# Kernel optimization log

Measured on AMD Instinct MI355X. Metric: run time of the kernel, lower is better.

## Reference

```python
import jax, jax.numpy as jnp
import numpy as np

B, N, C = 64, 197, 768
H = 12
N_TOK = 118
CUTOFF = 0.15


def setup_inputs() -> dict:
    key = jax.random.key(0)
    ks = jax.random.split(key, 6)
    s = 0.02
    return {
        "x": jax.random.normal(ks[0], (B, N, C), jnp.float32),
        "ln1_w": jnp.ones((C,), jnp.float32),
        "ln1_b": jnp.zeros((C,), jnp.float32),
        "qkv_w": jax.random.normal(ks[1], (3 * C, C), jnp.float32) * s,
        "proj_w": jax.random.normal(ks[2], (C, C), jnp.float32) * s,
        "proj_b": jnp.zeros((C,), jnp.float32),
        "gamma1": jnp.ones((C,), jnp.float32),
        "ln2_w": jnp.ones((C,), jnp.float32),
        "ln2_b": jnp.zeros((C,), jnp.float32),
        "fc1_w": jax.random.normal(ks[3], (4 * C, C), jnp.float32) * s,
        "fc1_b": jnp.zeros((4 * C,), jnp.float32),
        "fc2_w": jax.random.normal(ks[4], (C, 4 * C), jnp.float32) * s,
        "fc2_b": jnp.zeros((C,), jnp.float32),
        "gamma2": jnp.ones((C,), jnp.float32),
    }


def _ln(x, w, b, eps=1e-5):
    m = x.mean(-1, keepdims=True)
    v = ((x - m) ** 2).mean(-1, keepdims=True)
    return (x - m) / jnp.sqrt(v + eps) * w + b


def _attention(x, qkv_w, proj_w, proj_b):
    Bx, Nx, Cx = x.shape
    dh = Cx // H
    qkv = x @ qkv_w.T                                    # [B,N,3C]
    qk = qkv[:, :, : 2 * Cx].reshape(Bx, Nx, 2, H, dh).transpose(2, 0, 3, 1, 4)
    q, k = qk[0], qk[1]                                  # [B,H,N,dh]
    v = qkv[:, :, 2 * Cx :].reshape(Bx, Nx, H, dh).transpose(0, 2, 1, 3)
    attn = jax.nn.softmax((q * dh ** -0.5) @ k.transpose(0, 1, 3, 2), axis=-1)  # [B,H,N,N]
    out = (attn @ v).transpose(0, 2, 1, 3).reshape(Bx, Nx, Cx)
    return out @ proj_w.T + proj_b, attn


def _selector(x, attn, n_tokens, cutoff):
    # attention-weighted scores
    cls_aw = attn[:, :, 1:, 0].mean(-1)[..., None]        # [B,H,1]
    cls_attn = (attn[:, :, 0, 1:] * cls_aw).mean(1)       # [B,N-1]
    img_aw = attn[:, :, 0, 0][..., None]                  # [B,H,1]
    img_attn = (attn[:, :, 1:, 1:].mean(2) * img_aw).mean(1)
    token_attn = cls_attn + img_attn                      # [B,N-1]
    # FFT low-frequency-energy score (detached in original)
    img_token = jax.lax.stop_gradient(x[:, 1:].astype(jnp.float32).transpose(0, 2, 1))  # [B,C,N-1]
    f = jnp.fft.fft(img_token, axis=-1)
    amp = jnp.abs(f)
    pha = jnp.angle(f)
    L = img_token.shape[-1]
    d0 = (L * cutoff / 2.0) ** 2
    m0 = (L - 1) / 2.0
    grid = jnp.arange(L, dtype=jnp.float32)
    kernel = 1.0 - jnp.exp(-((grid - m0) ** 2) / (2.0 * d0))  # high-pass notch
    amp = amp * kernel
    f2 = amp * jnp.cos(pha) + 1j * amp * jnp.sin(pha)
    tok = jnp.fft.ifft(f2, axis=-1)                       # [B,C,N-1] complex
    token_lfe = jnp.abs(tok).sum(1) / jnp.abs(img_token).sum(1).mean(-1)[..., None]
    scores = token_lfe * token_attn                        # [B,N-1]
    _, idx = jax.lax.top_k(scores, n_tokens)               # [B,n_tokens]
    Cx = x.shape[-1]
    sav = jnp.take_along_axis(x[:, 1:], idx[:, :, None], axis=1)  # [B,n_tokens,C]
    return jnp.concatenate([x[:, 0:1], sav], axis=1)


def reference(x, ln1_w, ln1_b, qkv_w, proj_w, proj_b, gamma1,
              ln2_w, ln2_b, fc1_w, fc1_b, fc2_w, fc2_b, gamma2):
    x_msa, attn = _attention(_ln(x, ln1_w, ln1_b), qkv_w, proj_w, proj_b)
    x = gamma1 * x_msa + x
    x = _selector(x, attn, N_TOK, CUTOFF)                 # [B,1+N_TOK,C]
    h = _ln(x, ln2_w, ln2_b)
    h = jax.nn.gelu(h @ fc1_w.T + fc1_b, approximate=False)
    h = h @ fc2_w.T + fc2_b
    return gamma2 * h + x
```

## Files before the change

kernel.cpp:

```cpp
#include <hip/hip_runtime.h>
#include <math.h>

#define NTOK 197
#define NIMG 196
#define CDIM 768
#define NHEAD 12
#define HD 64
#define BATCH 64
#define NSEL 118
#define ROWS_FULL (BATCH*NTOK)
#define ROWS_SEL  (BATCH*(NSEL+1))

typedef short bf16x8 __attribute__((ext_vector_type(8)));
typedef float f32x4  __attribute__((ext_vector_type(4)));

#define GLDS(g, l) __builtin_amdgcn_global_load_lds( \
    (const __attribute__((address_space(1))) void*)(g), \
    (__attribute__((address_space(3))) void*)(l), 16, 0, 0)

__device__ __forceinline__ unsigned short f2bf(float f){
  union { float f; unsigned u; } v; v.f = f;
  unsigned r = v.u + 0x7FFF + ((v.u >> 16) & 1);
  return (unsigned short)(r >> 16);
}
__device__ __forceinline__ float bf2f(unsigned short h){
  union { unsigned u; float f; } v; v.u = ((unsigned)h) << 16; return v.f;
}

template<int OUT>
__global__ __launch_bounds__(256) void ln_kernel(
    const float* __restrict__ x, const float* __restrict__ w,
    const float* __restrict__ b, void* __restrict__ outv)
{
  const int row = blockIdx.x;
  const int t = threadIdx.x;
  const float* xr = x + (size_t)row * CDIM;
  float v0 = xr[t], v1 = xr[t+256], v2 = xr[t+512];
  float s = v0 + v1 + v2;
  __shared__ float red[4], red2[4];
  #pragma unroll
  for (int o=32;o>0;o>>=1) s += __shfl_down(s,o);
  if ((t&63)==0) red[t>>6] = s;
  __syncthreads();
  const float mean = (red[0]+red[1]+red[2]+red[3]) / 768.0f;
  const float d0=v0-mean, d1=v1-mean, d2=v2-mean;
  float vs = d0*d0 + d1*d1 + d2*d2;
  #pragma unroll
  for (int o=32;o>0;o>>=1) vs += __shfl_down(vs,o);
  if ((t&63)==0) red2[t>>6] = vs;
  __syncthreads();
  const float var = (red2[0]+red2[1]+red2[2]+red2[3]) / 768.0f;
  const float rstd = 1.0f / sqrtf(var + 1e-5f);
  const float o0 = d0*rstd*w[t]     + b[t];
  const float o1 = d1*rstd*w[t+256] + b[t+256];
  const float o2 = d2*rstd*w[t+512] + b[t+512];
  if (OUT == 0){
    float* orow = (float*)outv + (size_t)row * CDIM;
    orow[t] = o0; orow[t+256] = o1; orow[t+512] = o2;
  } else {
    unsigned short* orow = (unsigned short*)outv + (size_t)row * CDIM;
    orow[t] = f2bf(o0); orow[t+256] = f2bf(o1); orow[t+512] = f2bf(o2);
  }
}

__global__ __launch_bounds__(256) void ln_split3_kernel(
    const float* __restrict__ x, const float* __restrict__ w,
    const float* __restrict__ b, unsigned short* __restrict__ dst, size_t plane)
{
  const int row = blockIdx.x;
  const int t = threadIdx.x;
  const float* xr = x + (size_t)row * CDIM;
  float v0 = xr[t], v1 = xr[t+256], v2 = xr[t+512];
  float s = v0 + v1 + v2;
  __shared__ float red[4], red2[4];
  #pragma unroll
  for (int o=32;o>0;o>>=1) s += __shfl_down(s,o);
  if ((t&63)==0) red[t>>6] = s;
  __syncthreads();
  const float mean = (red[0]+red[1]+red[2]+red[3]) / 768.0f;
  const float d0=v0-mean, d1=v1-mean, d2=v2-mean;
  float vs = d0*d0 + d1*d1 + d2*d2;
  #pragma unroll
  for (int o=32;o>0;o>>=1) vs += __shfl_down(vs,o);
  if ((t&63)==0) red2[t>>6] = vs;
  __syncthreads();
  const float var = (red2[0]+red2[1]+red2[2]+red2[3]) / 768.0f;
  const float rstd = 1.0f / sqrtf(var + 1e-5f);
  const float ov[3] = { d0*rstd*w[t]     + b[t],
                        d1*rstd*w[t+256] + b[t+256],
                        d2*rstd*w[t+512] + b[t+512] };
  #pragma unroll
  for (int e=0;e<3;e++){
    const int col = t + e*256;
    const float f = ov[e];
    const unsigned short p0 = f2bf(f);
    const float r1 = f - bf2f(p0);
    const unsigned short p1 = f2bf(r1);
    const unsigned short p2 = f2bf(r1 - bf2f(p1));
    dst[(size_t)row*CDIM + col]             = p0;
    dst[plane + (size_t)row*CDIM + col]     = p1;
    dst[2*plane + (size_t)row*CDIM + col]   = p2;
  }
}

__global__ __launch_bounds__(256) void cvt_bf16_kernel(
    const float* __restrict__ src, unsigned short* __restrict__ dst, int n4)
{
  const int i = blockIdx.x*256 + threadIdx.x;
  if (i < n4){
    const float4 v = *(const float4*)(src + (size_t)i*4);
    dst[(size_t)i*4+0] = f2bf(v.x); dst[(size_t)i*4+1] = f2bf(v.y);
    dst[(size_t)i*4+2] = f2bf(v.z); dst[(size_t)i*4+3] = f2bf(v.w);
  }
}

__global__ __launch_bounds__(192) void cvt3_kernel(
    const float* __restrict__ w, unsigned short* __restrict__ W3, int K)
{
  const int n = blockIdx.x, t = threadIdx.x;
  const float4 v = *(const float4*)(w + (size_t)n*K + t*4);
  ushort4 hi, lo;
  hi.x = f2bf(v.x); lo.x = f2bf(v.x - bf2f(hi.x));
  hi.y = f2bf(v.y); lo.y = f2bf(v.y - bf2f(hi.y));
  hi.z = f2bf(v.z); lo.z = f2bf(v.z - bf2f(hi.z));
  hi.w = f2bf(v.w); lo.w = f2bf(v.w - bf2f(hi.w));
  *(ushort4*)(W3 + (size_t)n*2*K + t*4)     = hi;
  *(ushort4*)(W3 + (size_t)n*2*K + K + t*4) = lo;
}

__global__ __launch_bounds__(256) void cvt_split3_kernel(
    const float* __restrict__ src, unsigned short* __restrict__ dst,
    int n4, size_t plane)
{
  const int i = blockIdx.x*256 + threadIdx.x;
  if (i >= n4) return;
  const float4 v = *(const float4*)(src + (size_t)i*4);
  const float f[4] = {v.x, v.y, v.z, v.w};
  unsigned short p0[4], p1[4], p2[4];
  #pragma unroll
  for (int q=0;q<4;q++){
    p0[q] = f2bf(f[q]);
    const float r1 = f[q] - bf2f(p0[q]);
    p1[q] = f2bf(r1);
    const float r2 = r1 - bf2f(p1[q]);
    p2[q] = f2bf(r2);
  }
  *(ushort4*)(dst + (size_t)i*4)           = make_ushort4(p0[0],p0[1],p0[2],p0[3]);
  *(ushort4*)(dst + plane + (size_t)i*4)   = make_ushort4(p1[0],p1[1],p1[2],p1[3]);
  *(ushort4*)(dst + 2*plane + (size_t)i*4) = make_ushort4(p2[0],p2[1],p2[2],p2[3]);
}

__global__ __launch_bounds__(256) void gemm_f32_kernel(
    const float* __restrict__ A, const float* __restrict__ W,
    float* __restrict__ out, int M, int N, int K)
{
  __shared__ float As[16][132];
  __shared__ float Bs[16][132];
  const int t  = threadIdx.x;
  const int tx = t & 15, ty = t >> 4;
  const int m0 = blockIdx.x * 128, n0 = blockIdx.y * 128;
  const int lr = t >> 2, lc = (t & 3) << 2;
  float acc[2][2][4][4] = {{{{0.f}}}};
  const float4 z4 = make_float4(0.f,0.f,0.f,0.f);
  const int rowA0 = m0 + lr, rowA1 = m0 + 64 + lr;
  const size_t strA0 = (size_t)rowA0 * K, strA1 = (size_t)rowA1 * K;
  const size_t strW0 = (size_t)(n0+lr) * K, strW1 = (size_t)(n0+64+lr) * K;
  for (int k0=0; k0<K; k0+=16){
    float4 a0 = (rowA0 < M) ? *(const float4*)(A + strA0 + k0 + lc) : z4;
    float4 a1 = (rowA1 < M) ? *(const float4*)(A + strA1 + k0 + lc) : z4;
    float4 w0 = *(const float4*)(W + strW0 + k0 + lc);
    float4 w1 = *(const float4*)(W + strW1 + k0 + lc);
    __syncthreads();
    As[lc+0][lr]=a0.x; As[lc+1][lr]=a0.y; As[lc+2][lr]=a0.z; As[lc+3][lr]=a0.w;
    As[lc+0][64+lr]=a1.x; As[lc+1][64+lr]=a1.y; As[lc+2][64+lr]=a1.z; As[lc+3][64+lr]=a1.w;
    Bs[lc+0][lr]=w0.x; Bs[lc+1][lr]=w0.y; Bs[lc+2][lr]=w0.z; Bs[lc+3][lr]=w0.w;
    Bs[lc+0][64+lr]=w1.x; Bs[lc+1][64+lr]=w1.y; Bs[lc+2][64+lr]=w1.z; Bs[lc+3][64+lr]=w1.w;
    __syncthreads();
    #pragma unroll
    for (int k=0;k<16;k++){
      const float4 av0 = *(const float4*)&As[k][ty*4];
      const float4 av1 = *(const float4*)&As[k][64+ty*4];
      const float4 bv0 = *(const float4*)&Bs[k][tx*4];
      const float4 bv1 = *(const float4*)&Bs[k][64+tx*4];
      const float ar[2][4] = {{av0.x,av0.y,av0.z,av0.w},{av1.x,av1.y,av1.z,av1.w}};
      const float br[2][4] = {{bv0.x,bv0.y,bv0.z,bv0.w},{bv1.x,bv1.y,bv1.z,bv1.w}};
      #pragma unroll
      for (int ri=0;ri<2;ri++)
        #pragma unroll
        for (int i=0;i<4;i++)
          #pragma unroll
          for (int ci=0;ci<2;ci++)
            #pragma unroll
            for (int j=0;j<4;j++)
              acc[ri][ci][i][j] = fmaf(ar[ri][i], br[ci][j], acc[ri][ci][i][j]);
    }
  }
  #pragma unroll
  for (int ri=0;ri<2;ri++){
    #pragma unroll
    for (int i=0;i<4;i++){
      const int row = m0 + ri*64 + ty*4 + i;
      if (row >= M) continue;
      #pragma unroll
      for (int ci=0;ci<2;ci++){
        const int col = n0 + ci*64 + tx*4;
        *(float4*)(out + (size_t)row*N + col) =
          make_float4(acc[ri][ci][i][0],acc[ri][ci][i][1],acc[ri][ci][i][2],acc[ri][ci][i][3]);
      }
    }
  }
}

__global__ __launch_bounds__(512) void mfma_gemm6w_kernel(
    const unsigned short* __restrict__ A3, const unsigned short* __restrict__ W3,
    float* __restrict__ out, int M, int N, int K, size_t planeA, size_t planeW,
    int gx)
{
  __shared__ __align__(16) unsigned short As[3][64*64];
  __shared__ __align__(16) unsigned short Ws[256*64];
  const int nwg = gridDim.x;
  const int q8 = nwg >> 3, r8 = nwg & 7;
  const int xcd = blockIdx.x & 7, lid = blockIdx.x >> 3;
  const int swz = (xcd < r8) ? (xcd*(q8+1) + lid) : (r8*(q8+1) + (xcd-r8)*q8 + lid);
  const int bx = swz % gx, by = swz / gx;

  const int t = threadIdx.x;
  const int w = t >> 6, lane = t & 63;
  const int m0 = bx * 64, n0 = by * 256;
  const int wr = w >> 2, wc = w & 3;
  f32x4 acc[2][4];
  #pragma unroll
  for (int i=0;i<2;i++)
    #pragma unroll
    for (int j=0;j<4;j++){ acc[i][j][0]=0.f; acc[i][j][1]=0.f; acc[i][j][2]=0.f; acc[i][j][3]=0.f; }

  const int srow = lane >> 3;
  const int slot = lane & 7;
  const int scol = (slot ^ srow) * 8;
  const int aloc = w*8;
  const int wloc = w*32;
  const int fr = lane & 15;
  const int kg = lane >> 4;

  #define SEGW(NA)                                                            \
    _Pragma("unroll")                                                         \
    for (int ksub = 0; ksub < 2; ksub++){                                     \
      const int kbyte = ksub*64 + kg*16;                                      \
      bf16x8 b[4];                                                            \
      _Pragma("unroll")                                                       \
      for (int ni=0; ni<4; ni++){                                             \
        const int br = wc*64 + ni*16 + fr;                                    \
        b[ni] = *(const bf16x8*)(Ws + br*64 + ((kbyte ^ ((br&7)<<4)) >> 1));  \
      }                                                                       \
      _Pragma("unroll")                                                       \
      for (int p=0; p<NA; p++){                                               \
        bf16x8 a[2];                                                          \
        _Pragma("unroll")                                                     \
        for (int mi=0; mi<2; mi++){                                           \
          const int ar = wr*32 + mi*16 + fr;                                  \
          a[mi] = *(const bf16x8*)(As[p] + ar*64 + ((kbyte ^ ((ar&7)<<4)) >> 1)); \
        }                                                                     \
        _Pragma("unroll")                                                     \
        for (int mi=0; mi<2; mi++)                                            \
          _Pragma("unroll")                                                   \
          for (int ni=0; ni<4; ni++)                                          \
            acc[mi][ni] = __builtin_amdgcn_mfma_f32_16x16x32_bf16(a[mi], b[ni], acc[mi][ni], 0, 0, 0); \
      }                                                                       \
    }

  #define STAGE_W(P)                                                          \
    _Pragma("unroll")                                                         \
    for (int tt=0; tt<4; tt++){                                               \
      const int rl = wloc + tt*8;                                             \
      GLDS(W3 + (size_t)(P)*planeW + (size_t)(n0+rl+srow)*K + k0 + scol, Ws + rl*64); \
    }

  for (int k0 = 0; k0 < K; k0 += 64){
    __syncthreads();
    #pragma unroll
    for (int p=0; p<3; p++)
      GLDS(A3 + (size_t)p*planeA + (size_t)(m0+aloc+srow)*K + k0 + scol, As[p] + aloc*64);
    STAGE_W(0)
    __syncthreads();
    SEGW(3)
    __syncthreads();
    STAGE_W(1)
    __syncthreads();
    SEGW(2)
    __syncthreads();
    STAGE_W(2)
    __syncthreads();
    SEGW(1)
  }
  #undef SEGW
  #undef STAGE_W

  const int cL = lane & 15, rL = lane >> 4;
  #pragma unroll
  for (int mi=0; mi<2; mi++){
    #pragma unroll
    for (int ni=0; ni<4; ni++){
      const int col = n0 + wc*64 + ni*16 + cL;
      const int rowb = m0 + wr*32 + mi*16 + rL*4;
      #pragma unroll
      for (int r=0; r<4; r++){
        const int row = rowb + r;
        if (row >= M) continue;
        out[(size_t)row*N + col] = acc[mi][ni][r];
      }
    }
  }
}

template<int EPI>
__global__ __launch_bounds__(512) void mfma_gemm1w_kernel(
    const unsigned short* __restrict__ A, const unsigned short* __restrict__ W,
    const float* __restrict__ bias, const float* __restrict__ gamma,
    const float* __restrict__ resid, void* __restrict__ outv,
    int M, int N, int K, int gx)
{
  __shared__ __align__(16) unsigned short As[64*64];
  __shared__ __align__(16) unsigned short Ws[256*64];
  const int nwg = gridDim.x;
  const int q8 = nwg >> 3, r8 = nwg & 7;
  const int xcd = blockIdx.x & 7, lid = blockIdx.x >> 3;
  const int swz = (xcd < r8) ? (xcd*(q8+1) + lid) : (r8*(q8+1) + (xcd-r8)*q8 + lid);
  const int bx = swz % gx, by = swz / gx;

  const int t = threadIdx.x;
  const int w = t >> 6, lane = t & 63;
  const int m0 = bx * 64, n0 = by * 256;
  const int wr = w >> 2, wc = w & 3;
  f32x4 acc[2][4];
  #pragma unroll
  for (int i=0;i<2;i++)
    #pragma unroll
    for (int j=0;j<4;j++){ acc[i][j][0]=0.f; acc[i][j][1]=0.f; acc[i][j][2]=0.f; acc[i][j][3]=0.f; }

  const int srow = lane >> 3;
  const int slot = lane & 7;
  const int scol = (slot ^ srow) * 8;
  const int aloc = w*8;
  const int wloc = w*32;
  const int fr = lane & 15;
  const int kg = lane >> 4;

  for (int k0 = 0; k0 < K; k0 += 64){
    __syncthreads();
    GLDS(A + (size_t)(m0+aloc+srow)*K + k0 + scol, As + aloc*64);
    #pragma unroll
    for (int tt=0; tt<4; tt++){
      const int rl = wloc + tt*8;
      GLDS(W + (size_t)(n0+rl+srow)*K + k0 + scol, Ws + rl*64);
    }
    __syncthreads();
    #pragma unroll
    for (int ksub = 0; ksub < 2; ksub++){
      const int kbyte = ksub*64 + kg*16;
      bf16x8 b[4];
      #pragma unroll
      for (int ni=0; ni<4; ni++){
        const int br = wc*64 + ni*16 + fr;
        b[ni] = *(const bf16x8*)(Ws + br*64 + ((kbyte ^ ((br&7)<<4)) >> 1));
      }
      bf16x8 a[2];
      #pragma unroll
      for (int mi=0; mi<2; mi++){
        const int ar = wr*32 + mi*16 + fr;
        a[mi] = *(const bf16x8*)(As + ar*64 + ((kbyte ^ ((ar&7)<<4)) >> 1));
      }
      #pragma unroll
      for (int mi=0; mi<2; mi++)
        #pragma unroll
        for (int ni=0; ni<4; ni++)
          acc[mi][ni] = __builtin_amdgcn_mfma_f32_16x16x32_bf16(a[mi], b[ni], acc[mi][ni], 0, 0, 0);
    }
  }

  const int cL = lane & 15, rL = lane >> 4;
  #pragma unroll
  for (int mi=0; mi<2; mi++){
    #pragma unroll
    for (int ni=0; ni<4; ni++){
      const int col = n0 + wc*64 + ni*16 + cL;
      const int rowb = m0 + wr*32 + mi*16 + rL*4;
      const float bb = bias[col];
      #pragma unroll
      for (int r=0; r<4; r++){
        const int row = rowb + r;
        if (row >= M) continue;
        float v = acc[mi][ni][r] + bb;
        if (EPI == 2){
          v = 0.5f*v*(1.0f + erff(v*0.7071067811865475f));
          ((unsigned short*)outv)[(size_t)row*N + col] = f2bf(v);
        } else {
          v = gamma[col]*v + resid[(size_t)row*N + col];
          ((float*)outv)[(size_t)row*N + col] = v;
        }
      }
    }
  }
}

__global__ __launch_bounds__(512) void mfma_proj3_kernel(
    const unsigned short* __restrict__ A, const unsigned short* __restrict__ W,
    const float* __restrict__ bias, const float* __restrict__ gamma,
    const float* __restrict__ resid, float* __restrict__ out,
    int M, int N, int K, int gx)
{
  __shared__ __align__(16) unsigned short Ah[64*64], Al[64*64];
  __shared__ __align__(16) unsigned short Ws[256*64];
  const int nwg = gridDim.x;
  const int q8 = nwg >> 3, r8 = nwg & 7;
  const int xcd = blockIdx.x & 7, lid = blockIdx.x >> 3;
  const int swz = (xcd < r8) ? (xcd*(q8+1) + lid) : (r8*(q8+1) + (xcd-r8)*q8 + lid);
  const int bx = swz % gx, by = swz / gx;

  const int t = threadIdx.x;
  const int w = t >> 6, lane = t & 63;
  const int m0 = bx * 64, n0 = by * 256;
  const int wr = w >> 2, wc = w & 3;
  const int lda = 2*K;
  f32x4 acc[2][4];
  #pragma unroll
  for (int i=0;i<2;i++)
    #pragma unroll
    for (int j=0;j<4;j++){ acc[i][j][0]=0.f; acc[i][j][1]=0.f; acc[i][j][2]=0.f; acc[i][j][3]=0.f; }

  const int srow = lane >> 3;
  const int slot = lane & 7;
  const int scol = (slot ^ srow) * 8;
  const int aloc = w*8;
  const int wloc = w*32;
  const int fr = lane & 15;
  const int kg = lane >> 4;

  #define PSEG(NA)                                                            \
    _Pragma("unroll")                                                         \
    for (int ksub = 0; ksub < 2; ksub++){                                     \
      const int kbyte = ksub*64 + kg*16;                                      \
      bf16x8 b[4];                                                            \
      _Pragma("unroll")                                                       \
      for (int ni=0; ni<4; ni++){                                             \
        const int br = wc*64 + ni*16 + fr;                                    \
        b[ni] = *(const bf16x8*)(Ws + br*64 + ((kbyte ^ ((br&7)<<4)) >> 1));  \
      }                                                                       \
      _Pragma("unroll")                                                       \
      for (int mi=0; mi<2; mi++){                                             \
        const int ar = wr*32 + mi*16 + fr;                                    \
        const int ao = ar*64 + ((kbyte ^ ((ar&7)<<4)) >> 1);                  \
        bf16x8 ah = *(const bf16x8*)(Ah + ao);                                \
        _Pragma("unroll")                                                     \
        for (int ni=0; ni<4; ni++)                                            \
          acc[mi][ni] = __builtin_amdgcn_mfma_f32_16x16x32_bf16(ah, b[ni], acc[mi][ni], 0, 0, 0); \
        if (NA > 1){                                                          \
          bf16x8 al = *(const bf16x8*)(Al + ao);                              \
          _Pragma("unroll")                                                   \
          for (int ni=0; ni<4; ni++)                                          \
            acc[mi][ni] = __builtin_amdgcn_mfma_f32_16x16x32_bf16(al, b[ni], acc[mi][ni], 0, 0, 0); \
        }                                                                     \
      }                                                                       \
    }

  for (int k0 = 0; k0 < K; k0 += 64){
    __syncthreads();
    {
      const size_t abase = (size_t)(m0+aloc+srow)*lda + k0 + scol;
      GLDS(A + abase,     Ah + aloc*64);
      GLDS(A + abase + K, Al + aloc*64);
    }
    #pragma unroll
    for (int tt=0; tt<4; tt++){
      const int rl = wloc + tt*8;
      GLDS(W + (size_t)(n0+rl+srow)*lda + k0 + scol, Ws + rl*64);
    }
    __syncthreads();
    PSEG(2)
    __syncthreads();
    #pragma unroll
    for (int tt=0; tt<4; tt++){
      const int rl = wloc + tt*8;
      GLDS(W + (size_t)(n0+rl+srow)*lda + K + k0 + scol, Ws + rl*64);
    }
    __syncthreads();
    PSEG(1)
  }
  #undef PSEG

  const int cL = lane & 15, rL = lane >> 4;
  #pragma unroll
  for (int mi=0; mi<2; mi++){
    #pragma unroll
    for (int ni=0; ni<4; ni++){
      const int col = n0 + wc*64 + ni*16 + cL;
      const int rowb = m0 + wr*32 + mi*16 + rL*4;
      const float bb = bias[col];
      const float gg = gamma[col];
      #pragma unroll
      for (int r=0; r<4; r++){
        const int row = rowb + r;
        if (row >= M) continue;
        out[(size_t)row*N + col] = gg*(acc[mi][ni][r] + bb) + resid[(size_t)row*N + col];
      }
    }
  }
}

__global__ __launch_bounds__(256) void attn_flash_kernel(
    const float* __restrict__ qkv, double* __restrict__ mbuf,
    double* __restrict__ lbuf, unsigned short* __restrict__ msa3)
{
  __shared__ float Kt[NTOK][HD];
  __shared__ double q0s[HD];
  __shared__ float m0sh;
  __shared__ double red[4];
  __shared__ float l0f;
  const int bh = blockIdx.x;
  const int b = bh / NHEAD, h = bh % NHEAD;
  const float* basep = qkv + (size_t)b*NTOK*2304 + h*HD;
  for (int li=threadIdx.x; li<NTOK*16; li+=256){
    const int r = li >> 4, c4 = (li & 15) << 2;
    *(float4*)&Kt[r][c4] = *(const float4*)(basep + (size_t)r*2304 + 768 + c4);
  }
  if (threadIdx.x < 16){
    const float4 t4 = *(const float4*)(basep + threadIdx.x*4);
    q0s[threadIdx.x*4+0] = (double)t4.x*0.125; q0s[threadIdx.x*4+1] = (double)t4.y*0.125;
    q0s[threadIdx.x*4+2] = (double)t4.z*0.125; q0s[threadIdx.x*4+3] = (double)t4.w*0.125;
  }
  __syncthreads();
  const int i = threadIdx.x;
  float4 q[16];
  float4 o[16];
  float m = -INFINITY, l = 0.f;
  if (i < NTOK){
    #pragma unroll
    for (int dd=0; dd<16; dd++){
      float4 tq = *(const float4*)(basep + (size_t)i*2304 + dd*4);
      q[dd] = make_float4(tq.x*0.125f, tq.y*0.125f, tq.z*0.125f, tq.w*0.125f);
      o[dd] = make_float4(0.f,0.f,0.f,0.f);
    }
    for (int j=0;j<NTOK;j++){
      float s = 0.f;
      #pragma unroll
      for (int dd=0;dd<16;dd++){
        const float4 kk = *(const float4*)&Kt[j][dd*4];
        s = fmaf(q[dd].x,kk.x,s); s = fmaf(q[dd].y,kk.y,s);
        s = fmaf(q[dd].z,kk.z,s); s = fmaf(q[dd].w,kk.w,s);
      }
      const float mn = fmaxf(m, s);
      const float sc = expf(m - mn);
      const float p  = expf(s - mn);
      l = l*sc + p;
      if (sc != 1.0f){
        #pragma unroll
        for (int dd=0;dd<16;dd++){
          o[dd].x *= sc; o[dd].y *= sc; o[dd].z *= sc; o[dd].w *= sc;
        }
      }
      m = mn;
      const float* vrow = basep + (size_t)j*2304 + 1536;
      #pragma unroll
      for (int dd=0;dd<16;dd++){
        const float4 vv = *(const float4*)(vrow + dd*4);
        o[dd].x = fmaf(p,vv.x,o[dd].x); o[dd].y = fmaf(p,vv.y,o[dd].y);
        o[dd].z = fmaf(p,vv.z,o[dd].z); o[dd].w = fmaf(p,vv.w,o[dd].w);
      }
    }
    mbuf[bh*NTOK+i] = (double)m;
    if (i > 0) lbuf[bh*NTOK+i] = (double)(1.0f/l);
    if (i == 0) m0sh = m;
  }
  __syncthreads();
  double e = 0.0;
  if (i < NTOK){
    double s64 = 0.0;
    #pragma unroll
    for (int d=0; d<HD; d++) s64 = fma(q0s[d], (double)Kt[i][d], s64);
    e = exp(s64 - (double)m0sh);
  }
  #pragma unroll
  for (int o2=32;o2>0;o2>>=1) e += __shfl_down(e,o2);
  if ((i&63)==0) red[i>>6] = e;
  __syncthreads();
  if (i==0){
    const double l0 = 1.0/(red[0]+red[1]+red[2]+red[3]);
    lbuf[bh*NTOK] = l0;
    l0f = (float)l0;
  }
  __syncthreads();
  if (i >= NTOK) return;
  const float linv = (i == 0) ? l0f : (1.0f/l);
  unsigned short* orow = msa3 + ((size_t)b*NTOK + i)*1536 + h*HD;
  #pragma unroll
  for (int dd=0;dd<16;dd++){
    const float4 v = make_float4(o[dd].x*linv, o[dd].y*linv, o[dd].z*linv, o[dd].w*linv);
    ushort4 hi, lo;
    hi.x = f2bf(v.x); lo.x = f2bf(v.x - bf2f(hi.x));
    hi.y = f2bf(v.y); lo.y = f2bf(v.y - bf2f(hi.y));
    hi.z = f2bf(v.z); lo.z = f2bf(v.z - bf2f(hi.z));
    hi.w = f2bf(v.w); lo.w = f2bf(v.w - bf2f(hi.w));
    *(ushort4*)(orow + dd*4)       = hi;
    *(ushort4*)(orow + 768 + dd*4) = lo;
  }
}

__global__ __launch_bounds__(256) void attn_selp_kernel(
    const float* __restrict__ qkv, const double* __restrict__ mbuf,
    const double* __restrict__ lbuf, double* __restrict__ csp,
    double* __restrict__ e0buf)
{
  __shared__ float Qt[98][HD];
  __shared__ double q0s[HD];
  __shared__ float msf[98], lsf[98];
  const int bh   = blockIdx.x >> 1;
  const int half = blockIdx.x & 1;
  const int i2base = 1 + half*98;
  const int b = bh / NHEAD, h = bh % NHEAD;
  const float* basep = qkv + (size_t)b*NTOK*2304 + h*HD;
  for (int li=threadIdx.x; li<98*16; li+=256){
    const int r = li >> 4, c4 = (li & 15) << 2;
    float4 tq = *(const float4*)(basep + (size_t)(i2base + r)*2304 + c4);
    Qt[r][c4+0]=tq.x*0.125f; Qt[r][c4+1]=tq.y*0.125f;
    Qt[r][c4+2]=tq.z*0.125f; Qt[r][c4+3]=tq.w*0.125f;
  }
  if (half == 0 && threadIdx.x < 16){
    const float4 t4 = *(const float4*)(basep + threadIdx.x*4);
    q0s[threadIdx.x*4+0] = (double)t4.x*0.125; q0s[threadIdx.x*4+1] = (double)t4.y*0.125;
    q0s[threadIdx.x*4+2] = (double)t4.z*0.125; q0s[threadIdx.x*4+3] = (double)t4.w*0.125;
  }
  for (int li=threadIdx.x; li<98; li+=256){
    msf[li] = (float)mbuf[bh*NTOK + i2base + li];
    lsf[li] = (float)lbuf[bh*NTOK + i2base + li];
  }
  __syncthreads();
  const int j = threadIdx.x;
  if (j < NTOK){
    float4 kreg[16];
    #pragma unroll
    for (int dd=0;dd<16;dd++) kreg[dd] = *(const float4*)(basep + (size_t)j*2304 + 768 + dd*4);
    if (half == 0){
      const double m0d = mbuf[bh*NTOK];
      double s64 = 0.0;
      #pragma unroll
      for (int dd=0;dd<16;dd++){
        s64 = fma(q0s[dd*4+0], (double)kreg[dd].x, s64);
        s64 = fma(q0s[dd*4+1], (double)kreg[dd].y, s64);
        s64 = fma(q0s[dd*4+2], (double)kreg[dd].z, s64);
        s64 = fma(q0s[dd*4+3], (double)kreg[dd].w, s64);
      }
      e0buf[(size_t)bh*NTOK + j] = exp(s64 - m0d);
    }
    double colsum = 0.0;
    for (int r=0;r<98;r++){
      float s = 0.f;
      #pragma unroll
      for (int dd=0;dd<16;dd++){
        const float4 qq = *(const float4*)&Qt[r][dd*4];
        s = fmaf(qq.x,kreg[dd].x,s); s = fmaf(qq.y,kreg[dd].y,s);
        s = fmaf(qq.z,kreg[dd].z,s); s = fmaf(qq.w,kreg[dd].w,s);
      }
      colsum += (double)(expf(s - msf[r]) * lsf[r]);
    }
    csp[(size_t)blockIdx.x*NTOK + j] = colsum;
  }
}

__global__ __launch_bounds__(256) void attn_selc_kernel(
    const double* __restrict__ csp, const double* __restrict__ e0buf,
    double* __restrict__ ta_part)
{
  __shared__ double red[4];
  __shared__ double sh_cs0, sh_e00, sh_l0inv;
  const int bh = blockIdx.x;
  const int j = threadIdx.x;
  double colsum = 0.0, e0 = 0.0;
  if (j < NTOK){
    colsum = csp[(size_t)(bh*2)*NTOK + j] + csp[(size_t)(bh*2+1)*NTOK + j];
    e0 = e0buf[(size_t)bh*NTOK + j];
  }
  double e = e0;
  #pragma unroll
  for (int o=32;o>0;o>>=1) e += __shfl_down(e,o);
  if ((threadIdx.x&63)==0) red[threadIdx.x>>6] = e;
  __syncthreads();
  if (threadIdx.x == 0){
    sh_l0inv = 1.0/(red[0]+red[1]+red[2]+red[3]);
    sh_cs0 = colsum;
    sh_e00 = e0;
  }
  __syncthreads();
  if (j >= 1 && j < NTOK){
    const double row0 = e0 * sh_l0inv;
    const double r00  = sh_e00 * sh_l0inv;
    ta_part[(size_t)bh*NIMG + (j-1)] = row0 * (sh_cs0 / 196.0) + (colsum / 196.0) * r00;
  }
}

__global__ __launch_bounds__(256) void reduce_ta_kernel(
    const double* __restrict__ ta_part, double* __restrict__ token_attn)
{
  const int b = blockIdx.x, j = threadIdx.x;
  if (j < NIMG){
    double s = 0.0;
    for (int h=0; h<NHEAD; h++) s += ta_part[((size_t)b*NHEAD + h)*NIMG + j];
    token_attn[b*NIMG + j] = s / 12.0;
  }
}

__global__ __launch_bounds__(256) void circ_kernel(float* __restrict__ circ)
{
  const int d = blockIdx.x;
  const int g = threadIdx.x;
  __shared__ double rs[4], is[4];
  double re = 0.0, im = 0.0;
  if (g < NIMG){
    const double d0   = (196.0 * 0.15 / 2.0);
    const double twod = 2.0 * d0 * d0;
    const double gg = (double)g - 97.5;
    const double kg = 1.0 - exp(-(gg*gg)/twod);
    const int gd = (g*d) % NIMG;
    const double ang = 6.283185307179586476925286766559 * ((double)gd / 196.0);
    re = kg * cos(ang);
    im = kg * sin(ang);
  }
  #pragma unroll
  for (int o=32;o>0;o>>=1){ re += __shfl_down(re,o); im += __shfl_down(im,o); }
  if ((g&63)==0){ rs[g>>6] = re; is[g>>6] = im; }
  __syncthreads();
  if (g == 0){
    circ[d]        = (float)((rs[0]+rs[1]+rs[2]+rs[3]) / 196.0);
    circ[NIMG + d] = (float)((is[0]+is[1]+is[2]+is[3]) / 196.0);
  }
}

__global__ __launch_bounds__(256) void lfe_kernel(
    const float* __restrict__ x1, const float* __restrict__ circ,
    double* __restrict__ lfe_part, double* __restrict__ den_part)
{
  __shared__ float xs[NIMG][36];
  __shared__ float2 c2[NIMG];
  __shared__ double red[4];
  const int cg = blockIdx.x, b = blockIdx.y;
  const int c0 = cg * 32;
  for (int li=threadIdx.x; li<NIMG*32; li+=256){
    const int m = li >> 5, ch = li & 31;
    xs[m][ch] = x1[((size_t)b*NTOK + 1 + m)*CDIM + c0 + ch];
  }
  for (int li=threadIdx.x; li<NIMG; li+=256) c2[li] = make_float2(circ[li], circ[NIMG+li]);
  __syncthreads();
  const int n = threadIdx.x;
  double lfe_sum = 0.0, den_sum = 0.0;
  if (n < NIMG){
    #pragma unroll 1
    for (int g=0; g<4; g++){
      const int cc0 = g*8;
      float re[8] = {0,0,0,0,0,0,0,0};
      float im[8] = {0,0,0,0,0,0,0,0};
      int d = n;
      for (int mm=0; mm<NIMG; mm++){
        const float2 cc = c2[d];
        const float4 xa = *(const float4*)&xs[mm][cc0];
        const float4 xb = *(const float4*)&xs[mm][cc0+4];
        const float xv[8] = {xa.x,xa.y,xa.z,xa.w,xb.x,xb.y,xb.z,xb.w};
        #pragma unroll
        for (int q=0;q<8;q++){
          re[q] = fmaf(cc.x, xv[q], re[q]);
          im[q] = fmaf(cc.y, xv[q], im[q]);
        }
        d = (d==0) ? (NIMG-1) : (d-1);
      }
      #pragma unroll
      for (int q=0;q<8;q++) lfe_sum += (double)sqrtf(re[q]*re[q] + im[q]*im[q]);
    }
    #pragma unroll
    for (int q=0;q<8;q++){
      const float4 xv = *(const float4*)&xs[n][q*4];
      den_sum += (double)fabsf(xv.x)+(double)fabsf(xv.y)+(double)fabsf(xv.z)+(double)fabsf(xv.w);
    }
    lfe_part[((size_t)b*24 + cg)*NIMG + n] = lfe_sum;
  }
  double s = (n < NIMG) ? den_sum : 0.0;
  #pragma unroll
  for (int o=32;o>0;o>>=1) s += __shfl_down(s,o);
  if ((threadIdx.x & 63) == 0) red[threadIdx.x >> 6] = s;
  __syncthreads();
  if (threadIdx.x == 0) den_part[b*24 + cg] = red[0]+red[1]+red[2]+red[3];
}

__global__ __launch_bounds__(256) void scores_kernel(
    const double* __restrict__ lfe_part, const double* __restrict__ den_part,
    const double* __restrict__ token_attn, double* __restrict__ scores)
{
  const int b = blockIdx.x, n = threadIdx.x;
  if (n < NIMG){
    double num = 0.0;
    for (int cg=0; cg<24; cg++) num += lfe_part[((size_t)b*24 + cg)*NIMG + n];
    double den = 0.0;
    for (int cg=0; cg<24; cg++) den += den_part[b*24 + cg];
    const double tl = num / (den / 196.0);
    scores[b*NIMG + n] = tl * token_attn[b*NIMG + n];
  }
}

__global__ void topk_kernel(const double* __restrict__ scores, int* __restrict__ idx)
{
  __shared__ double w[NIMG];
  const int b = blockIdx.x, lane = threadIdx.x;
  for (int i=lane; i<NIMG; i+=64) w[i] = scores[b*NIMG + i];
  __syncthreads();
  for (int r=0; r<NSEL; r++){
    double bv = -INFINITY; int bi = NIMG;
    for (int i=lane; i<NIMG; i+=64){
      const double v = w[i];
      if (v > bv){ bv = v; bi = i; }
    }
    #pragma unroll
    for (int o=32;o>0;o>>=1){
      const double ov = __shfl_down(bv,o);
      const int    oi = __shfl_down(bi,o);
      if (ov > bv || (ov == bv && oi < bi)){ bv = ov; bi = oi; }
    }
    if (lane == 0){
      idx[b*NSEL + r] = bi;
      w[bi] = -INFINITY;
    }
    __syncthreads();
  }
}

__global__ void gather_kernel(const float* __restrict__ x1, const int* __restrict__ idx,
                              float* __restrict__ xsel)
{
  const int row = blockIdx.x;
  const int b = row / (NSEL+1), r = row % (NSEL+1);
  const int src = (r == 0) ? 0 : (1 + idx[b*NSEL + (r-1)]);
  const float4* s = (const float4*)(x1 + ((size_t)b*NTOK + src)*CDIM);
  float4* d = (float4*)(xsel + (size_t)row*CDIM);
  d[threadIdx.x] = s[threadIdx.x];
}

extern "C" void kernel_launch(void* const* d_in, const int* in_sizes, int n_in,
                              void* d_out, int out_size, void* d_ws, size_t ws_size,
                              hipStream_t stream)
{
  const float* x      = (const float*)d_in[0];
  const float* ln1_w  = (const float*)d_in[1];
  const float* ln1_b  = (const float*)d_in[2];
  const float* qkv_w  = (const float*)d_in[3];
  const float* proj_w = (const float*)d_in[4];
  const float* proj_b = (const float*)d_in[5];
  const float* gamma1 = (const float*)d_in[6];
  const float* ln2_w  = (const float*)d_in[7];
  const float* ln2_b  = (const float*)d_in[8];
  const float* fc1_w  = (const float*)d_in[9];
  const float* fc1_b  = (const float*)d_in[10];
  const float* fc2_w  = (const float*)d_in[11];
  const float* fc2_b  = (const float*)d_in[12];
  const float* gamma2 = (const float*)d_in[13];
  float* out = (float*)d_out;
  float* ws  = (float*)d_ws;

  float* R1 = ws;
  float* R2 = ws + 9732096;
  double* D = (double*)(ws + 9732096 + 29048832);
  double* mbuf = D;
  double* lbuf = mbuf + 151296;
  double* tap  = lbuf + 151296;
  double* ta   = tap  + 150528;
  double* lfep = ta   + 12544;
  double* denp = lfep + 301056;
  double* sc   = denp + 1536;
  float* circ  = (float*)(sc + 12544);
  int*   idxb  = (int*)(circ + 392);
  unsigned short* W3p = (unsigned short*)(ws + 40350472);
  unsigned short* WQ3 = (unsigned short*)(ws + 40940296);
  unsigned short* XQ3 = (unsigned short*)(ws + 43594504);
  const size_t NEED_BYTES = (size_t)58192648 * 4;

  double* csp   = lfep;
  double* e0buf = (double*)(ws + 40940296);

  float* xln  = R1;
  unsigned short* msa3 = (unsigned short*)R1;
  float* xsel = R1;
  float* qkv  = R2;
  float* x1   = R2;
  unsigned short* ln2o_bf = (unsigned short*)(R2 + 9682944);
  unsigned short* fc1w_bf = (unsigned short*)(R2 + 12632064);
  unsigned short* fc2w_bf = (unsigned short*)(R2 + 13811712);
  unsigned short* h1_bf   = (unsigned short*)(R2 + 14991360);

  if (ws_size >= NEED_BYTES){
    ln_split3_kernel<<<ROWS_FULL, 256, 0, stream>>>(x, ln1_w, ln1_b, XQ3, (size_t)9732096);
    cvt_split3_kernel<<<(442368+255)/256, 256, 0, stream>>>(qkv_w, WQ3, 442368, (size_t)1769472);
    mfma_gemm6w_kernel<<<197*9, 512, 0, stream>>>(XQ3, WQ3, qkv, ROWS_FULL, 2304, 768,
                                                  (size_t)9732096, (size_t)1769472, 197);
  } else {
    ln_kernel<0><<<ROWS_FULL, 256, 0, stream>>>(x, ln1_w, ln1_b, xln);
    gemm_f32_kernel<<<dim3(99,18), 256, 0, stream>>>(xln, qkv_w, qkv, ROWS_FULL, 2304, 768);
  }
  attn_flash_kernel<<<BATCH*NHEAD, 256, 0, stream>>>(qkv, mbuf, lbuf, msa3);
  attn_selp_kernel<<<BATCH*NHEAD*2, 256, 0, stream>>>(qkv, mbuf, lbuf, csp, e0buf);
  attn_selc_kernel<<<BATCH*NHEAD, 256, 0, stream>>>(csp, e0buf, tap);
  reduce_ta_kernel<<<BATCH, 256, 0, stream>>>(tap, ta);
  cvt3_kernel<<<CDIM, 192, 0, stream>>>(proj_w, W3p, CDIM);
  mfma_proj3_kernel<<<197*3, 512, 0, stream>>>(msa3, W3p, proj_b, gamma1, x,
                                               x1, ROWS_FULL, CDIM, CDIM, 197);
  cvt_bf16_kernel<<<2304, 256, 0, stream>>>(fc1_w, fc1w_bf, 589824);
  cvt_bf16_kernel<<<2304, 256, 0, stream>>>(fc2_w, fc2w_bf, 589824);
  circ_kernel<<<NIMG, 256, 0, stream>>>(circ);
  lfe_kernel<<<dim3(24, BATCH), 256, 0, stream>>>(x1, circ, lfep, denp);
  scores_kernel<<<BATCH, 256, 0, stream>>>(lfep, denp, ta, sc);
  topk_kernel<<<BATCH, 64, 0, stream>>>(sc, idxb);
  gather_kernel<<<ROWS_SEL, 192, 0, stream>>>(x1, idxb, xsel);
  ln_kernel<1><<<ROWS_SEL, 256, 0, stream>>>(xsel, ln2_w, ln2_b, ln2o_bf);
  mfma_gemm1w_kernel<2><<<119*12, 512, 0, stream>>>(ln2o_bf, fc1w_bf, fc1_b, nullptr,
                                                    nullptr, h1_bf, ROWS_SEL, 3072, 768, 119);
  mfma_gemm1w_kernel<3><<<119*3, 512, 0, stream>>>(h1_bf, fc2w_bf, fc2_b, gamma2,
                                                   xsel, out, ROWS_SEL, 768, 3072, 119);
}
```

Baseline: 1.128 ms.

## Split flash attention over two key halves with a separate combine kernel

```diff
diff --git a/kernel.cpp b/kernel.cpp
--- a/kernel.cpp
+++ b/kernel.cpp
@@ -604,6 +604,108 @@
   }
 }
 
+__global__ __launch_bounds__(256) void attn_flashp_kernel(
+    const float* __restrict__ qkv, float* __restrict__ opart,
+    float* __restrict__ mpart, float* __restrict__ lpart)
+{
+  __shared__ float Kt[99][HD];
+  const int bh   = blockIdx.x >> 1;
+  const int half = blockIdx.x & 1;
+  const int jbase = half ? 99 : 0;
+  const int jcnt  = half ? 98 : 99;
+  const int b = bh / NHEAD, h = bh % NHEAD;
+  const float* basep = qkv + (size_t)b*NTOK*2304 + h*HD;
+  for (int li=threadIdx.x; li<jcnt*16; li+=256){
+    const int r = li >> 4, c4 = (li & 15) << 2;
+    *(float4*)&Kt[r][c4] = *(const float4*)(basep + (size_t)(jbase+r)*2304 + 768 + c4);
+  }
+  __syncthreads();
+  const int i = threadIdx.x;
+  if (i >= NTOK) return;
+  float4 q[16], o[16];
+  #pragma unroll
+  for (int dd=0; dd<16; dd++){
+    float4 tq = *(const float4*)(basep + (size_t)i*2304 + dd*4);
+    q[dd] = make_float4(tq.x*0.125f, tq.y*0.125f, tq.z*0.125f, tq.w*0.125f);
+    o[dd] = make_float4(0.f,0.f,0.f,0.f);
+  }
+  float m = -INFINITY, l = 0.f;
+  for (int jj=0; jj<jcnt; jj++){
+    float s = 0.f;
+    #pragma unroll
+    for (int dd=0;dd<16;dd++){
+      const float4 kk = *(const float4*)&Kt[jj][dd*4];
+      s = fmaf(q[dd].x,kk.x,s); s = fmaf(q[dd].y,kk.y,s);
+      s = fmaf(q[dd].z,kk.z,s); s = fmaf(q[dd].w,kk.w,s);
+    }
+    const float mn = fmaxf(m, s);
+    const float sc = expf(m - mn);
+    const float p  = expf(s - mn);
+    l = l*sc + p;
+    if (sc != 1.0f){
+      #pragma unroll
+      for (int dd=0;dd<16;dd++){
+        o[dd].x *= sc; o[dd].y *= sc; o[dd].z *= sc; o[dd].w *= sc;
+      }
+    }
+    m = mn;
+    const float* vrow = basep + (size_t)(jbase+jj)*2304 + 1536;
+    #pragma unroll
+    for (int dd=0;dd<16;dd++){
+      const float4 vv = *(const float4*)(vrow + dd*4);
+      o[dd].x = fmaf(p,vv.x,o[dd].x); o[dd].y = fmaf(p,vv.y,o[dd].y);
+      o[dd].z = fmaf(p,vv.z,o[dd].z); o[dd].w = fmaf(p,vv.w,o[dd].w);
+    }
+  }
+  const size_t row = (size_t)blockIdx.x*NTOK + i;
+  mpart[row] = m;
+  lpart[row] = l;
+  float* orow = opart + row*64;
+  #pragma unroll
+  for (int dd=0;dd<16;dd++) *(float4*)(orow + dd*4) = o[dd];
+}
+
+__global__ __launch_bounds__(256) void attn_flashc_kernel(
+    const float* __restrict__ opart, const float* __restrict__ mpart,
+    const float* __restrict__ lpart, double* __restrict__ mbuf,
+    double* __restrict__ lbuf, unsigned short* __restrict__ msa3)
+{
+  const int bh = blockIdx.x;
+  const int b = bh / NHEAD, h = bh % NHEAD;
+  const int i = threadIdx.x;
+  if (i >= NTOK) return;
+  const size_t r0 = (size_t)(bh*2)*NTOK + i;
+  const size_t r1 = (size_t)(bh*2+1)*NTOK + i;
+  const float m0 = mpart[r0], m1 = mpart[r1];
+  const float l0 = lpart[r0], l1 = lpart[r1];
+  const float m = fmaxf(m0, m1);
+  const float sc0 = expf(m0 - m);
+  const float sc1 = expf(m1 - m);
+  const float l = l0*sc0 + l1*sc1;
+  const float linv = 1.0f / l;
+  mbuf[bh*NTOK+i] = (double)m;
+  lbuf[bh*NTOK+i] = (double)linv;
+  const float* o0 = opart + r0*64;
+  const float* o1 = opart + r1*64;
+  unsigned short* orow = msa3 + ((size_t)b*NTOK + i)*1536 + h*HD;
+  #pragma unroll
+  for (int dd=0;dd<16;dd++){
+    const float4 a = *(const float4*)(o0 + dd*4);
+    const float4 c = *(const float4*)(o1 + dd*4);
+    const float4 v = make_float4((a.x*sc0 + c.x*sc1)*linv,
+                                 (a.y*sc0 + c.y*sc1)*linv,
+                                 (a.z*sc0 + c.z*sc1)*linv,
+                                 (a.w*sc0 + c.w*sc1)*linv);
+    ushort4 hi, lo;
+    hi.x = f2bf(v.x); lo.x = f2bf(v.x - bf2f(hi.x));
+    hi.y = f2bf(v.y); lo.y = f2bf(v.y - bf2f(hi.y));
+    hi.z = f2bf(v.z); lo.z = f2bf(v.z - bf2f(hi.z));
+    hi.w = f2bf(v.w); lo.w = f2bf(v.w - bf2f(hi.w));
+    *(ushort4*)(orow + dd*4)       = hi;
+    *(ushort4*)(orow + 768 + dd*4) = lo;
+  }
+}
+
 __global__ __launch_bounds__(256) void attn_selp_kernel(
     const float* __restrict__ qkv, const double* __restrict__ mbuf,
     const double* __restrict__ lbuf, double* __restrict__ csp,
@@ -875,7 +977,11 @@
   unsigned short* W3p = (unsigned short*)(ws + 40350472);
   unsigned short* WQ3 = (unsigned short*)(ws + 40940296);
   unsigned short* XQ3 = (unsigned short*)(ws + 43594504);
-  const size_t NEED_BYTES = (size_t)58192648 * 4;
+  const size_t NEED_BYTES  = (size_t)58192648 * 4;
+  float* opart = ws + 58192648;
+  float* mpart = opart + 19365888;
+  float* lpart = mpart + 302592;
+  const size_t NEED2_BYTES = (size_t)78163720 * 4;
 
   double* csp   = lfep;
   double* e0buf = (double*)(ws + 40940296);
@@ -899,7 +1005,12 @@
     ln_kernel<0><<<ROWS_FULL, 256, 0, stream>>>(x, ln1_w, ln1_b, xln);
     gemm_f32_kernel<<<dim3(99,18), 256, 0, stream>>>(xln, qkv_w, qkv, ROWS_FULL, 2304, 768);
   }
-  attn_flash_kernel<<<BATCH*NHEAD, 256, 0, stream>>>(qkv, mbuf, lbuf, msa3);
+  if (ws_size >= NEED2_BYTES){
+    attn_flashp_kernel<<<BATCH*NHEAD*2, 256, 0, stream>>>(qkv, opart, mpart, lpart);
+    attn_flashc_kernel<<<BATCH*NHEAD, 256, 0, stream>>>(opart, mpart, lpart, mbuf, lbuf, msa3);
+  } else {
+    attn_flash_kernel<<<BATCH*NHEAD, 256, 0, stream>>>(qkv, mbuf, lbuf, msa3);
+  }
   attn_selp_kernel<<<BATCH*NHEAD*2, 256, 0, stream>>>(qkv, mbuf, lbuf, csp, e0buf);
   attn_selc_kernel<<<BATCH*NHEAD, 256, 0, stream>>>(csp, e0buf, tap);
   reduce_ta_kernel<<<BATCH, 256, 0, stream>>>(tap, ta);
```

New measurement: 1.126 ms. About the same (-0.2%).
